# Performance work log

Hardware: AMD Instinct MI355X
Metric: run time of the kernel (lower is better)

## Reference

```python
import jax, jax.numpy as jnp
import numpy as np

N_NODES = 50000
N_EDGES = 1600000
IN_DIM = 128
N_HEADS = 8
OUT_DIM = 16  # output_dim // n_heads = 128 // 8


def setup_inputs() -> dict:
    key = jax.random.key(0)
    ks = jax.random.split(key, 8)
    feature = jax.random.normal(ks[0], (N_NODES, IN_DIM), dtype=jnp.float32)
    edge_src = jax.random.randint(ks[1], (N_EDGES,), 0, N_NODES)
    edge_dst = jax.random.randint(ks[2], (N_EDGES,), 0, N_NODES)
    edge_weight = jax.random.uniform(ks[3], (N_EDGES,), dtype=jnp.float32)
    w_lin = jax.random.normal(ks[4], (IN_DIM, N_HEADS * OUT_DIM), dtype=jnp.float32) * 0.1
    att_l = jax.random.normal(ks[5], (N_HEADS, OUT_DIM), dtype=jnp.float32) * 0.1
    att_r = jax.random.normal(ks[6], (N_HEADS, OUT_DIM), dtype=jnp.float32) * 0.1
    w_res = jax.random.normal(ks[7], (IN_DIM, N_HEADS * OUT_DIM), dtype=jnp.float32) * 0.1
    return {"feature": feature, "edge_src": edge_src, "edge_dst": edge_dst,
            "edge_weight": edge_weight, "w_lin": w_lin, "att_l": att_l,
            "att_r": att_r, "w_res": w_res}


def reference(feature, edge_src, edge_dst, edge_weight, w_lin, att_l, att_r, w_res):
    N = feature.shape[0]
    H, C = att_l.shape
    # Linear projection -> [N, H, C]
    x = (feature @ w_lin).reshape(N, H, C)
    # Per-node attention logits [N, H]
    al = jnp.einsum('nhc,hc->nh', x, att_l)
    ar = jnp.einsum('nhc,hc->nh', x, att_r)
    # Per-edge logits: gather src/dst, weight, leaky-relu  [E, H]
    alpha = al[edge_src] + ar[edge_dst]
    alpha = edge_weight[:, None] * alpha
    alpha = jax.nn.leaky_relu(alpha, negative_slope=0.2)
    # Segment softmax over edges grouped by destination node
    m = jax.ops.segment_max(alpha, edge_dst, num_segments=N)  # [N, H]
    m = jnp.where(jnp.isfinite(m), m, 0.0)
    e = jnp.exp(alpha - m[edge_dst])
    denom = jax.ops.segment_sum(e, edge_dst, num_segments=N)  # [N, H]
    coef = e / denom[edge_dst]                                 # [E, H]
    # Message passing: gather src feats, weight by coef, scatter-sum to dst
    msg = x[edge_src] * coef[:, :, None]                       # [E, H, C]
    feat = jax.ops.segment_sum(msg, edge_dst, num_segments=N)  # [N, H, C]
    out = jax.nn.elu(feat).reshape(N, H * C)
    out = out + feature @ w_res  # residual branch
    return out
```

## Files before the change

### kernel.cpp

```cpp
#include <hip/hip_runtime.h>
#include <math.h>

#define IN_DIM 128
#define NH 8
#define OC 16
#define HC 128
#define BSTR 136
#define ECH 4096
#define NBINS_MAX 512
#define FSTR 132

typedef __attribute__((ext_vector_type(8))) short short8;
typedef __attribute__((ext_vector_type(4))) float f32x4;

__device__ __forceinline__ unsigned short bf16_rne(float f) {
  unsigned int u = __builtin_bit_cast(unsigned int, f);
  u += 0x7FFFu + ((u >> 16) & 1u);
  return (unsigned short)(u >> 16);
}
__device__ __forceinline__ float bf16_to_f(unsigned short h) {
  unsigned int u = ((unsigned int)h) << 16;
  return __builtin_bit_cast(float, u);
}

__global__ __launch_bounds__(256) void k1_fused(const float* __restrict__ feature,
                                                const float* __restrict__ w_lin,
                                                const float* __restrict__ w_res,
                                                const float* __restrict__ att_l,
                                                const float* __restrict__ att_r,
                                                unsigned char* __restrict__ x8,
                                                float* __restrict__ sscale,
                                                float* __restrict__ al,
                                                float* __restrict__ ar,
                                                float* __restrict__ out,
                                                int* __restrict__ bin_cursor, int N) {
  __shared__ unsigned short BL[HC * BSTR];
  __shared__ unsigned short BR[HC * BSTR];
  __shared__ unsigned short WH[16 * BSTR];
  __shared__ unsigned short WL[16 * BSTR];
  const int t = threadIdx.x;
  if (blockIdx.x == 0) {
    bin_cursor[t] = 0;
    bin_cursor[t + 256] = 0;
  }
  for (int i = t; i < IN_DIM * HC; i += 256) {
    const int r = i >> 7, c = i & 127;
    BL[c * BSTR + r] = bf16_rne(w_lin[i]);
    BR[c * BSTR + r] = bf16_rne(w_res[i]);
  }
#pragma unroll
  for (int j = 0; j < 8; ++j) {
    const int idx = t * 8 + j;
    const int k = idx >> 4, c = idx & 15;
    const int h8 = c & 7;
    const float* __restrict__ av = ((c < 8) ? att_l : att_r) + h8 * OC;
    const float* __restrict__ wr = w_lin + k * HC + h8 * OC;
    float acc = 0.f;
#pragma unroll
    for (int oc = 0; oc < 16; ++oc) acc = fmaf(wr[oc], av[oc], acc);
    const unsigned short hi = bf16_rne(acc);
    WH[c * BSTR + k] = hi;
    WL[c * BSTR + k] = bf16_rne(acc - bf16_to_f(hi));
  }
  __syncthreads();

  const int wave = t >> 6, lane = t & 63;
  const int n16 = lane & 15, quad = lane >> 4;
  const int nStrips = (N + 15) >> 4;

  for (int strip = blockIdx.x * 4 + wave; strip < nStrips; strip += gridDim.x * 4) {
    const int row0 = strip * 16;
    const int arow = row0 + n16;
    const float* __restrict__ ap =
        feature + (size_t)((arow < N) ? arow : 0) * IN_DIM + quad * 8;
    short8 ahi[4], alo[4];
#pragma unroll
    for (int ks = 0; ks < 4; ++ks) {
      const float4 f0 = *(const float4*)(ap + ks * 32);
      const float4 f1 = *(const float4*)(ap + ks * 32 + 4);
      const float fv[8] = {f0.x, f0.y, f0.z, f0.w, f1.x, f1.y, f1.z, f1.w};
      short8 h, l;
#pragma unroll
      for (int j = 0; j < 8; ++j) {
        const unsigned short hh = bf16_rne(fv[j]);
        h[j] = (short)hh;
        l[j] = (short)bf16_rne(fv[j] - bf16_to_f(hh));
      }
      ahi[ks] = h;
      alo[ks] = l;
    }
    f32x4 xacc[8];
#pragma unroll
    for (int u = 0; u < 8; ++u) xacc[u] = (f32x4){0.f, 0.f, 0.f, 0.f};
#pragma unroll
    for (int ks = 0; ks < 4; ++ks) {
#pragma unroll
      for (int u = 0; u < 8; ++u) {
        const int boff = (u * 16 + n16) * BSTR + ks * 32 + quad * 8;
        const short8 bh = *(const short8*)&BL[boff];
        xacc[u] = __builtin_amdgcn_mfma_f32_16x16x32_bf16(ahi[ks], bh, xacc[u], 0, 0, 0);
        xacc[u] = __builtin_amdgcn_mfma_f32_16x16x32_bf16(alo[ks], bh, xacc[u], 0, 0, 0);
      }
    }
    {
      f32x4 accA = {0.f, 0.f, 0.f, 0.f};
#pragma unroll
      for (int ks = 0; ks < 4; ++ks) {
        const int boff = n16 * BSTR + ks * 32 + quad * 8;
        const short8 wh = *(const short8*)&WH[boff];
        const short8 wl = *(const short8*)&WL[boff];
        accA = __builtin_amdgcn_mfma_f32_16x16x32_bf16(ahi[ks], wh, accA, 0, 0, 0);
        accA = __builtin_amdgcn_mfma_f32_16x16x32_bf16(alo[ks], wh, accA, 0, 0, 0);
        accA = __builtin_amdgcn_mfma_f32_16x16x32_bf16(ahi[ks], wl, accA, 0, 0, 0);
      }
#pragma unroll
      for (int r = 0; r < 4; ++r) {
        const int rr = row0 + quad * 4 + r;
        if (rr < N) {
          if (n16 < 8) al[(size_t)rr * NH + n16] = accA[r];
          else         ar[(size_t)rr * NH + (n16 - 8)] = accA[r];
        }
      }
    }
    float m[4];
#pragma unroll
    for (int r = 0; r < 4; ++r) {
      float mm = 0.f;
#pragma unroll
      for (int u = 0; u < 8; ++u) mm = fmaxf(mm, fabsf(xacc[u][r]));
      mm = fmaxf(mm, __shfl_xor(mm, 1));
      mm = fmaxf(mm, __shfl_xor(mm, 2));
      mm = fmaxf(mm, __shfl_xor(mm, 4));
      mm = fmaxf(mm, __shfl_xor(mm, 8));
      m[r] = mm;
    }
#pragma unroll
    for (int r = 0; r < 4; ++r) {
      const int rr = row0 + quad * 4 + r;
      if (rr < N) {
        const float inv = (m[r] > 0.f) ? 127.f / m[r] : 0.f;
#pragma unroll
        for (int u = 0; u < 8; ++u) {
          const int q8 = (int)rintf(xacc[u][r] * inv) + 128;
          x8[(size_t)rr * HC + u * 16 + n16] = (unsigned char)q8;
        }
        if (n16 == 0) sscale[rr] = (m[r] > 0.f) ? m[r] / 127.f : 0.f;
      }
    }
#pragma unroll
    for (int cg = 0; cg < 2; ++cg) {
      f32x4 acc[4] = {{0.f,0.f,0.f,0.f},{0.f,0.f,0.f,0.f},{0.f,0.f,0.f,0.f},{0.f,0.f,0.f,0.f}};
#pragma unroll
      for (int ks = 0; ks < 4; ++ks) {
#pragma unroll
        for (int j = 0; j < 4; ++j) {
          const int boff = ((cg * 4 + j) * 16 + n16) * BSTR + ks * 32 + quad * 8;
          const short8 bh = *(const short8*)&BR[boff];
          acc[j] = __builtin_amdgcn_mfma_f32_16x16x32_bf16(ahi[ks], bh, acc[j], 0, 0, 0);
          acc[j] = __builtin_amdgcn_mfma_f32_16x16x32_bf16(alo[ks], bh, acc[j], 0, 0, 0);
        }
      }
#pragma unroll
      for (int j = 0; j < 4; ++j) {
        const int colo = (cg * 4 + j) * 16 + n16;
#pragma unroll
        for (int r = 0; r < 4; ++r) {
          const int rr = row0 + quad * 4 + r;
          if (rr < N) out[(size_t)rr * HC + colo] = acc[j][r];
        }
      }
    }
  }
}

__global__ __launch_bounds__(1024) void kb1_scatter(const int* __restrict__ esrc,
                                                    const int* __restrict__ edst,
                                                    const float* __restrict__ ew,
                                                    int* __restrict__ bin_cursor,
                                                    uint2* __restrict__ tmp,
                                                    int E, int nbins, int cap) {
  __shared__ int cnt[NBINS_MAX];
  __shared__ int gbase[NBINS_MAX];
  const int t = threadIdx.x;
  if (t < NBINS_MAX) cnt[t] = 0;
  __syncthreads();
  const int base = blockIdx.x * ECH;
  uint2 v[4];
  int bj[4], sj[4];
#pragma unroll
  for (int j = 0; j < 4; ++j) {
    const int e = base + j * 1024 + t;
    bj[j] = -1;
    if (e < E) {
      const int d = edst[e];
      v[j] = make_uint2((unsigned)esrc[e] | ((unsigned)(d & 127) << 16),
                        __float_as_uint(ew[e]));
      bj[j] = d >> 7;
      sj[j] = atomicAdd(&cnt[bj[j]], 1);
    }
  }
  __syncthreads();
  for (int b = t; b < nbins; b += 1024) {
    const int own = cnt[b];
    if (own > 0) gbase[b] = atomicAdd(&bin_cursor[b], own);
  }
  __syncthreads();
#pragma unroll
  for (int j = 0; j < 4; ++j)
    if (bj[j] >= 0) {
      const int p = gbase[bj[j]] + sj[j];
      if (p >= 0 && p < cap) tmp[(size_t)bj[j] * cap + p] = v[j];
    }
}

__global__ __launch_bounds__(1024) void kb3_sort(const uint2* __restrict__ tmp,
                                                 const int* __restrict__ bin_cursor,
                                                 uint2* __restrict__ packed,
                                                 int* __restrict__ row_start,
                                                 int cap, int nbins, int N) {
  const int b = blockIdx.x, t = threadIdx.x;
  const int M = bin_cursor[b];
  __shared__ int redw[16];
  int part = 0;
  for (int i = t; i < b; i += 1024) part += bin_cursor[i];
#pragma unroll
  for (int o = 32; o >= 1; o >>= 1) part += __shfl_xor(part, o);
  if ((t & 63) == 0) redw[t >> 6] = part;
  __syncthreads();
  int gstart = 0;
#pragma unroll
  for (int w = 0; w < 16; ++w) gstart += redw[w];
  if (b == nbins - 1 && t == 0) row_start[N] = gstart + M;

  const uint2* __restrict__ src = tmp + (size_t)b * cap;
  __shared__ int cnt[128];
  __shared__ int cur[128];
  __shared__ int s[128];
  if (t < 128) cnt[t] = 0;
  __syncthreads();
  for (int i = t; i < M; i += 1024) atomicAdd(&cnt[src[i].x >> 16], 1);
  __syncthreads();
  if (t < 128) s[t] = cnt[t];
  __syncthreads();
  for (int o = 1; o < 128; o <<= 1) {
    int a = 0;
    if (t < 128 && t >= o) a = s[t - o];
    __syncthreads();
    if (t < 128) s[t] += a;
    __syncthreads();
  }
  if (t < 128) {
    const int ex = s[t] - cnt[t];
    cur[t] = gstart + ex;
    const int node = b * 128 + t;
    if (node < N) row_start[node] = gstart + ex;
  }
  __syncthreads();
  for (int i = t; i < M; i += 1024) {
    const uint2 v = src[i];
    const int pos = atomicAdd(&cur[v.x >> 16], 1);
    packed[pos] = make_uint2(v.x & 0xFFFFu, v.y);
  }
}

__global__ __launch_bounds__(64) void k5_agg(const unsigned char* __restrict__ x8,
                                             const float* __restrict__ s,
                                             const uint2* __restrict__ packed,
                                             const int* __restrict__ row_start,
                                             const float* __restrict__ al,
                                             const float* __restrict__ ar,
                                             float* __restrict__ out, int N) {
  const int n = blockIdx.x;
  const int l = threadIdx.x;
  const int s0 = row_start[n];
  const int En = row_start[n + 1] - s0;
  if (En == 0) return;
  __shared__ int sbuf[64];
  __shared__ float wbuf[64];
  __shared__ float scbuf[64];
  __shared__ float fred[8 * FSTR];
  const int h = l & 7;
  const int g = l >> 3;
  const int ch0 = h * 16;

  const float arn = ar[(size_t)n * NH + h];
  float dpart = 0.f;
  float facsum = 0.f;
  float f[16];
#pragma unroll
  for (int j = 0; j < 16; ++j) f[j] = 0.f;

  for (int base = 0; base < En; base += 64) {
    const int cnt = min(64, En - base);
    __syncthreads();
    if (l < cnt) {
      const uint2 p = packed[s0 + base + l];
      const int src = (int)p.x;
      sbuf[l] = src;
      wbuf[l] = __uint_as_float(p.y);
      scbuf[l] = s[src];
    }
    __syncthreads();
    for (int i = g; i < cnt; i += 8) {
      const int src = sbuf[i];
      float a = wbuf[i] * (al[(size_t)src * NH + h] + arn);
      a = (a > 0.f) ? a : 0.2f * a;
      const float e = __expf(a);
      dpart += e;
      const float fac = e * scbuf[i];
      facsum += fac;
      const int4 qw = *(const int4*)(x8 + (size_t)src * HC + ch0);
      const unsigned ux = (unsigned)qw.x, uy = (unsigned)qw.y;
      const unsigned uz = (unsigned)qw.z, uw = (unsigned)qw.w;
      f[0]  = fmaf(fac, (float)(ux & 0xFFu),         f[0]);
      f[1]  = fmaf(fac, (float)((ux >> 8) & 0xFFu),  f[1]);
      f[2]  = fmaf(fac, (float)((ux >> 16) & 0xFFu), f[2]);
      f[3]  = fmaf(fac, (float)(ux >> 24),           f[3]);
      f[4]  = fmaf(fac, (float)(uy & 0xFFu),         f[4]);
      f[5]  = fmaf(fac, (float)((uy >> 8) & 0xFFu),  f[5]);
      f[6]  = fmaf(fac, (float)((uy >> 16) & 0xFFu), f[6]);
      f[7]  = fmaf(fac, (float)(uy >> 24),           f[7]);
      f[8]  = fmaf(fac, (float)(uz & 0xFFu),         f[8]);
      f[9]  = fmaf(fac, (float)((uz >> 8) & 0xFFu),  f[9]);
      f[10] = fmaf(fac, (float)((uz >> 16) & 0xFFu), f[10]);
      f[11] = fmaf(fac, (float)(uz >> 24),           f[11]);
      f[12] = fmaf(fac, (float)(uw & 0xFFu),         f[12]);
      f[13] = fmaf(fac, (float)((uw >> 8) & 0xFFu),  f[13]);
      f[14] = fmaf(fac, (float)((uw >> 16) & 0xFFu), f[14]);
      f[15] = fmaf(fac, (float)(uw >> 24),           f[15]);
    }
  }
  dpart += __shfl_xor(dpart, 8);
  dpart += __shfl_xor(dpart, 16);
  dpart += __shfl_xor(dpart, 32);
  facsum += __shfl_xor(facsum, 8);
  facsum += __shfl_xor(facsum, 16);
  facsum += __shfl_xor(facsum, 32);
#pragma unroll
  for (int q = 0; q < 4; ++q) {
    const f32x4 v = {f[q * 4 + 0], f[q * 4 + 1], f[q * 4 + 2], f[q * 4 + 3]};
    *(f32x4*)&fred[g * FSTR + ch0 + q * 4] = v;
  }
  __syncthreads();
  float a0 = 0.f, a1 = 0.f;
#pragma unroll
  for (int gg = 0; gg < 8; ++gg) {
    const float2 v = *(const float2*)&fred[gg * FSTR + 2 * l];
    a0 += v.x;
    a1 += v.y;
  }
  const float dH = __shfl(dpart, l >> 3);
  const float fsH = __shfl(facsum, l >> 3);
  const float inv = 1.f / dH;
  float f0 = (a0 - 128.f * fsH) * inv;
  float f1 = (a1 - 128.f * fsH) * inv;
  f0 = (f0 > 0.f) ? f0 : (__expf(f0) - 1.f);
  f1 = (f1 > 0.f) ? f1 : (__expf(f1) - 1.f);
  float2 o = *(float2*)&out[(size_t)n * HC + 2 * l];
  o.x += f0;
  o.y += f1;
  *(float2*)&out[(size_t)n * HC + 2 * l] = o;
}

extern "C" void kernel_launch(void* const* d_in, const int* in_sizes, int n_in,
                              void* d_out, int out_size, void* d_ws, size_t ws_size,
                              hipStream_t stream) {
  const float* feature = (const float*)d_in[0];
  const int* esrc = (const int*)d_in[1];
  const int* edst = (const int*)d_in[2];
  const float* ew = (const float*)d_in[3];
  const float* w_lin = (const float*)d_in[4];
  const float* att_l = (const float*)d_in[5];
  const float* att_r = (const float*)d_in[6];
  const float* w_res = (const float*)d_in[7];
  float* out = (float*)d_out;

  const int N = in_sizes[0] / IN_DIM;
  const int E = in_sizes[1];
  const int nbins = (N + 127) >> 7;
  int cap = (E + nbins - 1) / nbins;
  cap = cap + cap / 4 + 512;
  cap = (cap + 63) & ~63;
  const int nch = (E + ECH - 1) / ECH;

  char* ws = (char*)d_ws;
  size_t off = 0;
  auto alloc = [&](size_t bytes) {
    void* p = ws + off;
    off = (off + bytes + 255) & ~(size_t)255;
    return p;
  };
  uint2* tmp = (uint2*)alloc((size_t)nbins * cap * sizeof(uint2));
  unsigned char* x8 = (unsigned char*)alloc((size_t)N * HC);
  float* sscale = (float*)alloc((size_t)N * sizeof(float));
  float* al = (float*)alloc((size_t)N * NH * sizeof(float));
  float* ar = (float*)alloc((size_t)N * NH * sizeof(float));
  int* row_start = (int*)alloc((size_t)(N + 1) * sizeof(int));
  int* bin_cursor = (int*)alloc((size_t)NBINS_MAX * sizeof(int));
  uint2* packed = (uint2*)alloc((size_t)E * sizeof(uint2));

  k1_fused<<<512, 256, 0, stream>>>(feature, w_lin, w_res, att_l, att_r,
                                    x8, sscale, al, ar, out, bin_cursor, N);
  kb1_scatter<<<nch, 1024, 0, stream>>>(esrc, edst, ew, bin_cursor, tmp, E, nbins, cap);
  kb3_sort<<<nbins, 1024, 0, stream>>>(tmp, bin_cursor, packed, row_start, cap, nbins, N);
  k5_agg<<<N, 64, 0, stream>>>(x8, sscale, packed, row_start, al, ar, out, N);
}
```

Baseline: 193.3 us.

## Pack quantized features, bf16 src logits and scale into one row; shrink bins

```diff
diff --git a/kernel.cpp b/kernel.cpp
--- a/kernel.cpp
+++ b/kernel.cpp
@@ -6,9 +6,13 @@
 #define OC 16
 #define HC 128
 #define BSTR 136
-#define ECH 4096
-#define NBINS_MAX 512
+#define ECH 2048
+#define BINSZ 64
+#define NBINS_MAX 1024
 #define FSTR 132
+#define XROW 160
+#define AL_OFF 128
+#define S_OFF 144
 
 typedef __attribute__((ext_vector_type(8))) short short8;
 typedef __attribute__((ext_vector_type(4))) float f32x4;
@@ -28,9 +32,7 @@
                                                 const float* __restrict__ w_res,
                                                 const float* __restrict__ att_l,
                                                 const float* __restrict__ att_r,
-                                                unsigned char* __restrict__ x8,
-                                                float* __restrict__ sscale,
-                                                float* __restrict__ al,
+                                                unsigned char* __restrict__ xr,
                                                 float* __restrict__ ar,
                                                 float* __restrict__ out,
                                                 int* __restrict__ bin_cursor, int N) {
@@ -42,6 +44,8 @@
   if (blockIdx.x == 0) {
     bin_cursor[t] = 0;
     bin_cursor[t + 256] = 0;
+    bin_cursor[t + 512] = 0;
+    bin_cursor[t + 768] = 0;
   }
   for (int i = t; i < IN_DIM * HC; i += 256) {
     const int r = i >> 7, c = i & 127;
@@ -117,8 +121,12 @@
       for (int r = 0; r < 4; ++r) {
         const int rr = row0 + quad * 4 + r;
         if (rr < N) {
-          if (n16 < 8) al[(size_t)rr * NH + n16] = accA[r];
-          else         ar[(size_t)rr * NH + (n16 - 8)] = accA[r];
+          if (n16 < 8) {
+            *(unsigned short*)(xr + (size_t)rr * XROW + AL_OFF + n16 * 2) =
+                bf16_rne(accA[r]);
+          } else {
+            ar[(size_t)rr * NH + (n16 - 8)] = accA[r];
+          }
         }
       }
     }
@@ -142,9 +150,10 @@
 #pragma unroll
         for (int u = 0; u < 8; ++u) {
           const int q8 = (int)rintf(xacc[u][r] * inv) + 128;
-          x8[(size_t)rr * HC + u * 16 + n16] = (unsigned char)q8;
+          xr[(size_t)rr * XROW + u * 16 + n16] = (unsigned char)q8;
         }
-        if (n16 == 0) sscale[rr] = (m[r] > 0.f) ? m[r] / 127.f : 0.f;
+        if (n16 == 0)
+          *(float*)(xr + (size_t)rr * XROW + S_OFF) = (m[r] > 0.f) ? m[r] / 127.f : 0.f;
       }
     }
 #pragma unroll
@@ -182,20 +191,20 @@
   __shared__ int cnt[NBINS_MAX];
   __shared__ int gbase[NBINS_MAX];
   const int t = threadIdx.x;
-  if (t < NBINS_MAX) cnt[t] = 0;
+  cnt[t] = 0;
   __syncthreads();
   const int base = blockIdx.x * ECH;
-  uint2 v[4];
-  int bj[4], sj[4];
-#pragma unroll
-  for (int j = 0; j < 4; ++j) {
+  uint2 v[2];
+  int bj[2], sj[2];
+#pragma unroll
+  for (int j = 0; j < 2; ++j) {
     const int e = base + j * 1024 + t;
     bj[j] = -1;
     if (e < E) {
       const int d = edst[e];
-      v[j] = make_uint2((unsigned)esrc[e] | ((unsigned)(d & 127) << 16),
+      v[j] = make_uint2((unsigned)esrc[e] | ((unsigned)(d & (BINSZ - 1)) << 16),
                         __float_as_uint(ew[e]));
-      bj[j] = d >> 7;
+      bj[j] = d >> 6;
       sj[j] = atomicAdd(&cnt[bj[j]], 1);
     }
   }
@@ -206,7 +215,7 @@
   }
   __syncthreads();
 #pragma unroll
-  for (int j = 0; j < 4; ++j)
+  for (int j = 0; j < 2; ++j)
     if (bj[j] >= 0) {
       const int p = gbase[bj[j]] + sj[j];
       if (p >= 0 && p < cap) tmp[(size_t)bj[j] * cap + p] = v[j];
@@ -233,26 +242,26 @@
   if (b == nbins - 1 && t == 0) row_start[N] = gstart + M;
 
   const uint2* __restrict__ src = tmp + (size_t)b * cap;
-  __shared__ int cnt[128];
-  __shared__ int cur[128];
-  __shared__ int s[128];
-  if (t < 128) cnt[t] = 0;
+  __shared__ int cnt[BINSZ];
+  __shared__ int cur[BINSZ];
+  __shared__ int s[BINSZ];
+  if (t < BINSZ) cnt[t] = 0;
   __syncthreads();
   for (int i = t; i < M; i += 1024) atomicAdd(&cnt[src[i].x >> 16], 1);
   __syncthreads();
-  if (t < 128) s[t] = cnt[t];
-  __syncthreads();
-  for (int o = 1; o < 128; o <<= 1) {
+  if (t < BINSZ) s[t] = cnt[t];
+  __syncthreads();
+  for (int o = 1; o < BINSZ; o <<= 1) {
     int a = 0;
-    if (t < 128 && t >= o) a = s[t - o];
+    if (t < BINSZ && t >= o) a = s[t - o];
     __syncthreads();
-    if (t < 128) s[t] += a;
+    if (t < BINSZ) s[t] += a;
     __syncthreads();
   }
-  if (t < 128) {
+  if (t < BINSZ) {
     const int ex = s[t] - cnt[t];
     cur[t] = gstart + ex;
-    const int node = b * 128 + t;
+    const int node = b * BINSZ + t;
     if (node < N) row_start[node] = gstart + ex;
   }
   __syncthreads();
@@ -263,11 +272,9 @@
   }
 }
 
-__global__ __launch_bounds__(64) void k5_agg(const unsigned char* __restrict__ x8,
-                                             const float* __restrict__ s,
+__global__ __launch_bounds__(64) void k5_agg(const unsigned char* __restrict__ xr,
                                              const uint2* __restrict__ packed,
                                              const int* __restrict__ row_start,
-                                             const float* __restrict__ al,
                                              const float* __restrict__ ar,
                                              float* __restrict__ out, int N) {
   const int n = blockIdx.x;
@@ -298,18 +305,20 @@
       const int src = (int)p.x;
       sbuf[l] = src;
       wbuf[l] = __uint_as_float(p.y);
-      scbuf[l] = s[src];
+      scbuf[l] = *(const float*)(xr + (size_t)src * XROW + S_OFF);
     }
     __syncthreads();
     for (int i = g; i < cnt; i += 8) {
       const int src = sbuf[i];
-      float a = wbuf[i] * (al[(size_t)src * NH + h] + arn);
+      const unsigned char* __restrict__ rp = xr + (size_t)src * XROW;
+      const float aln = bf16_to_f(*(const unsigned short*)(rp + AL_OFF + (h << 1)));
+      float a = wbuf[i] * (aln + arn);
       a = (a > 0.f) ? a : 0.2f * a;
       const float e = __expf(a);
       dpart += e;
       const float fac = e * scbuf[i];
       facsum += fac;
-      const int4 qw = *(const int4*)(x8 + (size_t)src * HC + ch0);
+      const int4 qw = *(const int4*)(rp + ch0);
       const unsigned ux = (unsigned)qw.x, uy = (unsigned)qw.y;
       const unsigned uz = (unsigned)qw.z, uw = (unsigned)qw.w;
       f[0]  = fmaf(fac, (float)(ux & 0xFFu),         f[0]);
@@ -377,7 +386,7 @@
 
   const int N = in_sizes[0] / IN_DIM;
   const int E = in_sizes[1];
-  const int nbins = (N + 127) >> 7;
+  const int nbins = (N + BINSZ - 1) / BINSZ;
   int cap = (E + nbins - 1) / nbins;
   cap = cap + cap / 4 + 512;
   cap = (cap + 63) & ~63;
@@ -391,17 +400,15 @@
     return p;
   };
   uint2* tmp = (uint2*)alloc((size_t)nbins * cap * sizeof(uint2));
-  unsigned char* x8 = (unsigned char*)alloc((size_t)N * HC);
-  float* sscale = (float*)alloc((size_t)N * sizeof(float));
-  float* al = (float*)alloc((size_t)N * NH * sizeof(float));
+  unsigned char* xr = (unsigned char*)alloc((size_t)N * XROW);
   float* ar = (float*)alloc((size_t)N * NH * sizeof(float));
   int* row_start = (int*)alloc((size_t)(N + 1) * sizeof(int));
   int* bin_cursor = (int*)alloc((size_t)NBINS_MAX * sizeof(int));
   uint2* packed = (uint2*)alloc((size_t)E * sizeof(uint2));
 
   k1_fused<<<512, 256, 0, stream>>>(feature, w_lin, w_res, att_l, att_r,
-                                    x8, sscale, al, ar, out, bin_cursor, N);
+                                    xr, ar, out, bin_cursor, N);
   kb1_scatter<<<nch, 1024, 0, stream>>>(esrc, edst, ew, bin_cursor, tmp, E, nbins, cap);
   kb3_sort<<<nbins, 1024, 0, stream>>>(tmp, bin_cursor, packed, row_start, cap, nbins, N);
-  k5_agg<<<N, 64, 0, stream>>>(x8, sscale, packed, row_start, al, ar, out, N);
-}
+  k5_agg<<<N, 64, 0, stream>>>(xr, packed, row_start, ar, out, N);
+}
```

Result: slower. 207.0 us (+7.1%).
